# Kernel tuning notes

Measured on AMD Instinct MI355X. Metric: run time of the kernel, lower is better.

The kernel has to match this reference:

```python
import jax, jax.numpy as jnp
import numpy as np

N, D, E, TOP_K = 2048, 512, 16, 2
HID = 4 * D
EPS = 1e-10


def setup_inputs() -> dict:
    key = jax.random.key(0)
    ks = jax.random.split(key, 8)
    s = 0.02
    return {
        "x": jax.random.normal(ks[0], (N, D), dtype=jnp.float32),
        "w_norm": jnp.ones((D,), dtype=jnp.float32),
        "Wr": jax.random.normal(ks[1], (D, E), dtype=jnp.float32) * s,
        "br": jnp.zeros((E,), dtype=jnp.float32),
        "W1": jax.random.normal(ks[2], (E, D, HID), dtype=jnp.float32) * s,
        "b1": jnp.zeros((E, HID), dtype=jnp.float32),
        "W2": jax.random.normal(ks[3], (E, HID, D), dtype=jnp.float32) * s,
        "b2": jnp.zeros((E, D), dtype=jnp.float32),
    }


def reference(x, w_norm, Wr, br, W1, b1, W2, b2):
    res = x
    # RMSNorm over feature dim (dim=1 in the torch code for 2D input)
    rms = jnp.sqrt(jnp.mean(x * x, axis=1, keepdims=True) + EPS)
    xn = w_norm * (x / rms)
    # Router: top-k over expert logits, softmax over the k selected logits
    logits = xn @ Wr + br                      # [N, E]
    top_p, top_i = jax.lax.top_k(logits, TOP_K)  # [N, k]
    top_p = jax.nn.softmax(top_p, axis=-1)
    # Dense per-token expert weights [N, E] (top-k indices are distinct)
    weight = jnp.zeros((x.shape[0], E), dtype=x.dtype)
    weight = weight.at[jnp.arange(x.shape[0])[:, None], top_i].add(top_p)
    # All-expert FFN (dense reference for the routed dispatch)
    h = jnp.einsum("nd,edh->enh", xn, W1) + b1[:, None, :]   # [E, N, 4D]
    y = jnp.einsum("enh,ehd->end", jax.nn.silu(h), W2) + b2[:, None, :]  # [E, N, D]
    out = jnp.einsum("end,ne->nd", y, weight)
    return out + res
```

## Files before the change

kernel.cpp:

```cpp
#include <hip/hip_runtime.h>

#define N_TOK 2048
#define DIM   512
#define NEXP  16
#define HID   2048
#define NSLOT (N_TOK*2)

typedef __attribute__((ext_vector_type(8))) short short8;
typedef __attribute__((ext_vector_type(4))) float floatx4;

__device__ __forceinline__ ushort f2bf(float f) {
    union { float f; unsigned u; } c; c.f = f;
    unsigned u = c.u;
    unsigned r = (u + 0x7fffu + ((u >> 16) & 1u)) >> 16;
    return (ushort)r;
}

__device__ __forceinline__ void gl_lds16(const void* g, void* l) {
    __builtin_amdgcn_global_load_lds(
        (const __attribute__((address_space(1))) unsigned int*)g,
        (__attribute__((address_space(3))) unsigned int*)l, 16, 0, 0);
}

__global__ __launch_bounds__(256)
void transpose_convert(const float* __restrict__ src, ushort* __restrict__ dst,
                       int K, int Nn)
{
    const int NT = Nn >> 6, KT = K >> 6;
    int bx = blockIdx.x;
    const int nt = bx % NT; bx /= NT;
    const int kt = bx % KT; bx /= KT;
    const int e  = bx;

    __shared__ float Ls[64 * 65];
    const int t = threadIdx.x;

    const float* sp = src + ((size_t)e * K + kt * 64) * Nn + nt * 64;
#pragma unroll
    for (int i = 0; i < 4; i++) {
        const int k  = (t >> 4) + i * 16;
        const int c4 = (t & 15) * 4;
        const float4 v = *(const float4*)(sp + (size_t)k * Nn + c4);
        Ls[k * 65 + c4 + 0] = v.x;
        Ls[k * 65 + c4 + 1] = v.y;
        Ls[k * 65 + c4 + 2] = v.z;
        Ls[k * 65 + c4 + 3] = v.w;
    }
    __syncthreads();

    ushort* dp = dst + ((size_t)e * Nn + nt * 64) * K + kt * 64;
#pragma unroll
    for (int i = 0; i < 2; i++) {
        const int n = (t >> 3) + i * 32;
        const int c = t & 7;
        unsigned w[4];
#pragma unroll
        for (int q = 0; q < 4; q++) {
            const unsigned lo = f2bf(Ls[(c * 8 + q * 2 + 0) * 65 + n]);
            const unsigned hi = f2bf(Ls[(c * 8 + q * 2 + 1) * 65 + n]);
            w[q] = lo | (hi << 16);
        }
        uint4 o = make_uint4(w[0], w[1], w[2], w[3]);
        *(uint4*)(dp + (size_t)n * K + c * 8) = o;
    }
}

__global__ __launch_bounds__(256)
void router_fused(const float* __restrict__ x, const float* __restrict__ w_norm,
                  const float* __restrict__ Wr, const float* __restrict__ br,
                  ushort* __restrict__ xn, int2* __restrict__ rec_e,
                  float2* __restrict__ rec_w)
{
    __shared__ float xs[16][516];
    __shared__ float wrT[16][516];

    const int tid  = threadIdx.x;
    const int wave = tid >> 6, lane = tid & 63;
    const int tblk = blockIdx.x * 16;

#pragma unroll
    for (int k = 0; k < 32; k++) {
        const int idx = tid + k * 256;
        wrT[idx & 15][idx >> 4] = Wr[idx];
    }

    const float4* wnp = (const float4*)w_norm;
    const float4 wa = wnp[lane], wb = wnp[lane + 64];
#pragma unroll
    for (int i = 0; i < 4; i++) {
        const int tl = wave * 4 + i, t = tblk + tl;
        const float4* xp = (const float4*)(x + (size_t)t * DIM);
        const float4 a = xp[lane], b = xp[lane + 64];
        float ss = a.x*a.x + a.y*a.y + a.z*a.z + a.w*a.w
                 + b.x*b.x + b.y*b.y + b.z*b.z + b.w*b.w;
#pragma unroll
        for (int m = 32; m >= 1; m >>= 1) ss += __shfl_xor(ss, m, 64);
        const float rinv = 1.f / sqrtf(ss * (1.f / (float)DIM) + 1e-10f);
        float4 na, nb;
        na.x = a.x * wa.x * rinv; na.y = a.y * wa.y * rinv;
        na.z = a.z * wa.z * rinv; na.w = a.w * wa.w * rinv;
        nb.x = b.x * wb.x * rinv; nb.y = b.y * wb.y * rinv;
        nb.z = b.z * wb.z * rinv; nb.w = b.w * wb.w * rinv;
        *(float4*)&xs[tl][lane * 4]       = na;
        *(float4*)&xs[tl][256 + lane * 4] = nb;
        ushort4 ua, ub;
        ua.x = f2bf(na.x); ua.y = f2bf(na.y); ua.z = f2bf(na.z); ua.w = f2bf(na.w);
        ub.x = f2bf(nb.x); ub.y = f2bf(nb.y); ub.z = f2bf(nb.z); ub.w = f2bf(nb.w);
        ushort4* xo = (ushort4*)(xn + (size_t)t * DIM);
        xo[lane] = ua; xo[lane + 64] = ub;
    }
    __syncthreads();

    const int tl = tid >> 4, e = tid & 15;
    const int t = tblk + tl;
    float acc = 0.f;
#pragma unroll 4
    for (int d = 0; d < DIM; d += 4) {
        const float4 xv = *(const float4*)&xs[tl][d];
        const float4 wv = *(const float4*)&wrT[e][d];
        acc += xv.x * wv.x + xv.y * wv.y + xv.z * wv.z + xv.w * wv.w;
    }
    const float v = acc + br[e];

    float m0 = v; int i0 = e; float m1 = -1e30f; int i1 = 16;
#pragma unroll
    for (int msk = 1; msk < 16; msk <<= 1) {
        const float om0 = __shfl_xor(m0, msk, 64); const int oi0 = __shfl_xor(i0, msk, 64);
        const float om1 = __shfl_xor(m1, msk, 64); const int oi1 = __shfl_xor(i1, msk, 64);
        const bool bf_ = (om0 > m0) || (om0 == m0 && oi0 < i0);
        const float t0m = bf_ ? om0 : m0; const int t0i = bf_ ? oi0 : i0;
        const float l0m = bf_ ? m0 : om0; const int l0i = bf_ ? i0 : oi0;
        const bool b2_ = (om1 > m1) || (om1 == m1 && oi1 < i1);
        const float t2m = b2_ ? om1 : m1; const int t2i = b2_ ? oi1 : i1;
        const bool lw = (l0m > t2m) || (l0m == t2m && l0i < t2i);
        m0 = t0m; i0 = t0i;
        m1 = lw ? l0m : t2m; i1 = lw ? l0i : t2i;
    }
    if (e == 0) {
        const float ex = expf(m1 - m0);
        const float w0 = 1.f / (1.f + ex);
        rec_e[t] = make_int2(i0, i1);
        rec_w[t] = make_float2(w0, ex * w0);
    }
}

__global__ __launch_bounds__(1024)
void plan_kernel(const int2* __restrict__ rec_e, int* __restrict__ cnt,
                 int* __restrict__ off, int* __restrict__ tok_of_slot,
                 int* __restrict__ rec_slot)
{
    __shared__ int soff[17];
    const int e = threadIdx.x >> 6;
    const int lane = threadIdx.x & 63;

    int total = 0;
    for (int c = 0; c < N_TOK / 64; c++) {
        const int2 er = rec_e[c * 64 + lane];
        const bool hit = (er.x == e) || (er.y == e);
        total += __popcll(__ballot(hit));
    }
    if (lane == 0) soff[e + 1] = total;
    __syncthreads();
    if (threadIdx.x == 0) {
        soff[0] = 0;
        for (int q = 1; q <= 16; q++) soff[q] += soff[q - 1];
    }
    __syncthreads();
    int base = soff[e];
    if (lane == 0) { cnt[e] = soff[e + 1] - base; off[e] = base; }

    for (int c = 0; c < N_TOK / 64; c++) {
        const int t = c * 64 + lane;
        const int2 er = rec_e[t];
        const bool hit = (er.x == e) || (er.y == e);
        const unsigned long long b = __ballot(hit);
        if (hit) {
            const int slot = base + __popcll(b & ((1ull << lane) - 1ull));
            tok_of_slot[slot] = t;
            const int which = (er.y == e) ? 1 : 0;
            rec_slot[t * 2 + which] = slot;
        }
        base += __popcll(b);
    }
}

template<int MODE>
__global__ __launch_bounds__(512)
void gemm_expert(const ushort* __restrict__ A, int a_stride,
                 const ushort* __restrict__ WT, int wt_k,
                 const float* __restrict__ bias,
                 const int* __restrict__ cnt, const int* __restrict__ off,
                 const int* __restrict__ tok_of_slot,
                 ushort* __restrict__ hout, float* __restrict__ yout)
{
    const int flat = blockIdx.x + (blockIdx.y << 4);
    const int x = flat & 7;
    const int g = flat >> 3;
    int e, mt, nb, z;
    if (MODE == 0) {
        e  = x + ((g >> 6) << 3);
        const int r = g & 63;
        nb = r & 15; mt = r >> 4; z = 0;
    } else {
        const int G = ((g >> 4) << 3) + x;
        e = G >> 2; z = G & 3;
        const int idx = g & 15;
        mt = idx >> 2; nb = idx & 3;
    }

    const int count = cnt[e];
    if (mt * 128 >= count) return;
    const int base = off[e];
    const int rows = min(128, count - mt * 128);
    const int n0   = nb * 128;
    const int Nn   = (MODE == 0) ? HID : DIM;
    const int kbeg = (MODE == 0) ? 0 : (z * 512);
    float* yp = (MODE == 0) ? nullptr : (yout + (size_t)z * NSLOT * DIM);

    __shared__ __align__(16) ushort As[2][128 * 64];
    __shared__ __align__(16) ushort Bs[2][128 * 64];
    __shared__ int toks[128];

    const int tid = threadIdx.x;
    if (tid < 128) {
        const int r = tid < rows ? tid : rows - 1;
        const int slot = base + mt * 128 + r;
        toks[tid] = (MODE == 0) ? tok_of_slot[slot] : slot;
    }
    __syncthreads();

    const int lane = tid & 63;
    const int wid  = tid >> 6;
    const int wm = wid >> 2, wn = wid & 3;
    const int fr = lane & 15, fg = lane >> 4;

    const int lrow = lane >> 3;
    const int sch  = (lane & 7) ^ lrow;

    const ushort* aptr[2];
    const ushort* bptr[2];
    const ushort* wbase = WT + (size_t)e * Nn * wt_k + (size_t)n0 * wt_k;
#pragma unroll
    for (int j = 0; j < 2; j++) {
        const int s = wid * 2 + j;
        aptr[j] = A + (size_t)toks[s * 8 + lrow] * a_stride + sch * 8;
        bptr[j] = wbase + (size_t)(s * 8 + lrow) * wt_k + sch * 8;
    }

    floatx4 acc[4][2];
#pragma unroll
    for (int mi = 0; mi < 4; mi++)
#pragma unroll
        for (int ni = 0; ni < 2; ni++)
#pragma unroll
            for (int r = 0; r < 4; r++) acc[mi][ni][r] = 0.f;

#define STAGE(pb, k0)                                                        \
    do {                                                                     \
        _Pragma("unroll")                                                    \
        for (int j = 0; j < 2; j++)                                          \
            gl_lds16(aptr[j] + (k0), (void*)(&As[pb][(wid * 2 + j) * 512])); \
        _Pragma("unroll")                                                    \
        for (int j = 0; j < 2; j++)                                          \
            gl_lds16(bptr[j] + (k0), (void*)(&Bs[pb][(wid * 2 + j) * 512])); \
    } while (0)

    int cur = 0;
    STAGE(0, kbeg);

    for (int kt = 0; kt < 8; kt++) {
        if (kt < 7) {
            STAGE(cur ^ 1, kbeg + (kt + 1) * 64);
            asm volatile("s_waitcnt vmcnt(4)" ::: "memory");
        } else {
            asm volatile("s_waitcnt vmcnt(0)" ::: "memory");
        }
        __builtin_amdgcn_s_barrier();
        __builtin_amdgcn_sched_barrier(0);

        __builtin_amdgcn_s_setprio(1);
#pragma unroll
        for (int kh = 0; kh < 2; kh++) {
            const int co = ((kh * 4 + fg) ^ (fr & 7)) * 8;
            short8 af[4], bfr[2];
#pragma unroll
            for (int mi = 0; mi < 4; mi++)
                af[mi] = *(const short8*)&As[cur][(wm * 64 + mi * 16 + fr) * 64 + co];
#pragma unroll
            for (int ni = 0; ni < 2; ni++)
                bfr[ni] = *(const short8*)&Bs[cur][(wn * 32 + ni * 16 + fr) * 64 + co];
#pragma unroll
            for (int mi = 0; mi < 4; mi++)
#pragma unroll
                for (int ni = 0; ni < 2; ni++)
                    acc[mi][ni] = __builtin_amdgcn_mfma_f32_16x16x32_bf16(af[mi], bfr[ni], acc[mi][ni], 0, 0, 0);
        }
        __builtin_amdgcn_s_setprio(0);

        __builtin_amdgcn_sched_barrier(0);
        __builtin_amdgcn_s_barrier();
        cur ^= 1;
    }
#undef STAGE

#pragma unroll
    for (int ni = 0; ni < 2; ni++) {
        const int gn = n0 + wn * 32 + ni * 16 + fr;
        const float bv = (MODE == 0) ? bias[e * HID + gn] : 0.f;
#pragma unroll
        for (int mi = 0; mi < 4; mi++) {
#pragma unroll
            for (int r = 0; r < 4; r++) {
                const int lm = wm * 64 + mi * 16 + fg * 4 + r;
                if (lm < rows) {
                    const int slot = base + mt * 128 + lm;
                    float v = acc[mi][ni][r];
                    if (MODE == 0) {
                        v += bv;
                        v = v / (1.f + expf(-v));
                        hout[(size_t)slot * HID + gn] = f2bf(v);
                    } else {
                        yp[(size_t)slot * DIM + gn] = v;
                    }
                }
            }
        }
    }
}

__global__ __launch_bounds__(128)
void gather_kernel(const float* __restrict__ x, const float* __restrict__ ypart,
                   const float* __restrict__ b2,
                   const int2* __restrict__ rec_e, const float2* __restrict__ rec_w,
                   const int2* __restrict__ rec_slot, float* __restrict__ out)
{
    const int t = blockIdx.x;
    const int d4 = threadIdx.x * 4;
    const int2 ei = rec_e[t];
    const float2 w = rec_w[t];
    const int2 sl = rec_slot[t];
    const float4 xv  = *(const float4*)(x  + (size_t)t * DIM + d4);
    float4 s0 = make_float4(0.f, 0.f, 0.f, 0.f);
    float4 s1 = make_float4(0.f, 0.f, 0.f, 0.f);
#pragma unroll
    for (int kc = 0; kc < 4; kc++) {
        const float* yp = ypart + (size_t)kc * NSLOT * DIM;
        const float4 a = *(const float4*)(yp + (size_t)sl.x * DIM + d4);
        const float4 b = *(const float4*)(yp + (size_t)sl.y * DIM + d4);
        s0.x += a.x; s0.y += a.y; s0.z += a.z; s0.w += a.w;
        s1.x += b.x; s1.y += b.y; s1.z += b.z; s1.w += b.w;
    }
    const float4 b0  = *(const float4*)(b2 + (size_t)ei.x * DIM + d4);
    const float4 b1v = *(const float4*)(b2 + (size_t)ei.y * DIM + d4);
    float4 o;
    o.x = xv.x + w.x * (s0.x + b0.x) + w.y * (s1.x + b1v.x);
    o.y = xv.y + w.x * (s0.y + b0.y) + w.y * (s1.y + b1v.y);
    o.z = xv.z + w.x * (s0.z + b0.z) + w.y * (s1.z + b1v.z);
    o.w = xv.w + w.x * (s0.w + b0.w) + w.y * (s1.w + b1v.w);
    *(float4*)(out + (size_t)t * DIM + d4) = o;
}

extern "C" void kernel_launch(void* const* d_in, const int* in_sizes, int n_in,
                              void* d_out, int out_size, void* d_ws, size_t ws_size,
                              hipStream_t stream)
{
    const float* x  = (const float*)d_in[0];
    const float* wn = (const float*)d_in[1];
    const float* Wr = (const float*)d_in[2];
    const float* br = (const float*)d_in[3];
    const float* W1 = (const float*)d_in[4];
    const float* b1 = (const float*)d_in[5];
    const float* W2 = (const float*)d_in[6];
    const float* b2 = (const float*)d_in[7];
    float* out = (float*)d_out;

    char* ws = (char*)d_ws;
    ushort* W1T   = (ushort*)(ws);
    ushort* W2T   = (ushort*)(ws + (32u << 20));
    ushort* xn    = (ushort*)(ws + (64u << 20));
    ushort* h_buf = (ushort*)(ws + (66u << 20));
    float*  y_par = (float*) (ws + (82u << 20));
    char* p = ws + (114u << 20);
    int*    cnt         = (int*)p;    p += 256;
    int*    off         = (int*)p;    p += 256;
    int2*   rec_e       = (int2*)p;   p += N_TOK * 8;
    float2* rec_w       = (float2*)p; p += N_TOK * 8;
    int2*   rec_slot    = (int2*)p;   p += N_TOK * 8;
    int*    tok_of_slot = (int*)p;    p += NSLOT * 4;

    router_fused<<<N_TOK / 16, 256, 0, stream>>>(x, wn, Wr, br, xn, rec_e, rec_w);
    plan_kernel<<<1, 1024, 0, stream>>>(rec_e, cnt, off, tok_of_slot, (int*)rec_slot);

    transpose_convert<<<NEXP * 8 * 32, 256, 0, stream>>>(W1, W1T, DIM, HID);
    gemm_expert<0><<<dim3(16, 64), 512, 0, stream>>>(
        xn, DIM, W1T, DIM, b1, cnt, off, tok_of_slot, h_buf, nullptr);

    transpose_convert<<<NEXP * 32 * 8, 256, 0, stream>>>(W2, W2T, HID, DIM);
    gemm_expert<1><<<dim3(16, 64), 512, 0, stream>>>(
        h_buf, HID, W2T, HID, nullptr, cnt, off, nullptr, nullptr, y_par);

    gather_kernel<<<N_TOK, 128, 0, stream>>>(x, y_par, b2, rec_e, rec_w, rec_slot, out);
}
```

Before: 116.9 us.

## Double expert GEMM M-tile to 256 rows and store partial outputs in bf16

Expert GEMM blocks now cover 256 token rows instead of 128. Each wave computes a 64x64 sub-tile with a 4x4 MFMA accumulator array, and the grid is halved. The down-projection split-K partials are written as bf16 instead of fp32, and the gather kernel converts them back, which halves that intermediate traffic. SiLU switches to the fast __expf. The aim is better operand reuse and less memory traffic, at the cost of fewer active blocks, more LDS and registers per block, and slightly lower precision in the partial sums.

Result: slower. 126.8 us (+8.5%).

```diff
diff --git a/kernel.cpp b/kernel.cpp
--- a/kernel.cpp
+++ b/kernel.cpp
@@ -14,6 +14,10 @@
     unsigned u = c.u;
     unsigned r = (u + 0x7fffu + ((u >> 16) & 1u)) >> 16;
     return (ushort)r;
+}
+__device__ __forceinline__ float bf2f(ushort u) {
+    union { unsigned u; float f; } c; c.u = ((unsigned)u) << 16;
+    return c.f;
 }
 
 __device__ __forceinline__ void gl_lds16(const void* g, void* l) {
@@ -191,75 +195,79 @@
                  const float* __restrict__ bias,
                  const int* __restrict__ cnt, const int* __restrict__ off,
                  const int* __restrict__ tok_of_slot,
-                 ushort* __restrict__ hout, float* __restrict__ yout)
+                 ushort* __restrict__ hout, ushort* __restrict__ yout)
 {
     const int flat = blockIdx.x + (blockIdx.y << 4);
     const int x = flat & 7;
     const int g = flat >> 3;
     int e, mt, nb, z;
     if (MODE == 0) {
-        e  = x + ((g >> 6) << 3);
-        const int r = g & 63;
+        e  = x + ((g >> 5) << 3);
+        const int r = g & 31;
         nb = r & 15; mt = r >> 4; z = 0;
     } else {
-        const int G = ((g >> 4) << 3) + x;
+        const int G = ((g >> 3) << 3) + x;
         e = G >> 2; z = G & 3;
-        const int idx = g & 15;
+        const int idx = g & 7;
         mt = idx >> 2; nb = idx & 3;
     }
 
     const int count = cnt[e];
-    if (mt * 128 >= count) return;
+    if (mt * 256 >= count) return;
     const int base = off[e];
-    const int rows = min(128, count - mt * 128);
+    const int rows = min(256, count - mt * 256);
     const int n0   = nb * 128;
     const int Nn   = (MODE == 0) ? HID : DIM;
     const int kbeg = (MODE == 0) ? 0 : (z * 512);
-    float* yp = (MODE == 0) ? nullptr : (yout + (size_t)z * NSLOT * DIM);
-
-    __shared__ __align__(16) ushort As[2][128 * 64];
+    ushort* yp = (MODE == 0) ? nullptr : (yout + (size_t)z * NSLOT * DIM);
+
+    __shared__ __align__(16) ushort As[2][256 * 64];
     __shared__ __align__(16) ushort Bs[2][128 * 64];
-    __shared__ int toks[128];
+    __shared__ int toks[256];
 
     const int tid = threadIdx.x;
-    if (tid < 128) {
+    if (tid < 256) {
         const int r = tid < rows ? tid : rows - 1;
-        const int slot = base + mt * 128 + r;
+        const int slot = base + mt * 256 + r;
         toks[tid] = (MODE == 0) ? tok_of_slot[slot] : slot;
     }
     __syncthreads();
 
     const int lane = tid & 63;
     const int wid  = tid >> 6;
-    const int wm = wid >> 2, wn = wid & 3;
+    const int wm = wid >> 1, wn = wid & 1;
     const int fr = lane & 15, fg = lane >> 4;
 
     const int lrow = lane >> 3;
     const int sch  = (lane & 7) ^ lrow;
 
-    const ushort* aptr[2];
+    const ushort* aptr[4];
     const ushort* bptr[2];
     const ushort* wbase = WT + (size_t)e * Nn * wt_k + (size_t)n0 * wt_k;
 #pragma unroll
+    for (int j = 0; j < 4; j++) {
+        const int s = wid * 4 + j;
+        aptr[j] = A + (size_t)toks[s * 8 + lrow] * a_stride + sch * 8;
+    }
+#pragma unroll
     for (int j = 0; j < 2; j++) {
         const int s = wid * 2 + j;
-        aptr[j] = A + (size_t)toks[s * 8 + lrow] * a_stride + sch * 8;
         bptr[j] = wbase + (size_t)(s * 8 + lrow) * wt_k + sch * 8;
     }
 
-    floatx4 acc[4][2];
+    floatx4 acc[4][4];
 #pragma unroll
     for (int mi = 0; mi < 4; mi++)
 #pragma unroll
-        for (int ni = 0; ni < 2; ni++)
+        for (int ni = 0; ni < 4; ni++)
 #pragma unroll
             for (int r = 0; r < 4; r++) acc[mi][ni][r] = 0.f;
 
 #define STAGE(pb, k0)                                                        \
     do {                                                                     \
         _Pragma("unroll")                                                    \
-        for (int j = 0; j < 2; j++)                                          \
-            gl_lds16(aptr[j] + (k0), (void*)(&As[pb][(wid * 2 + j) * 512])); \
+        for (int j = 0; j < 4; j++)                                          \
+            gl_lds16(aptr[j] + (k0), (void*)(&As[pb][(wid * 4 + j) * 512])); \
         _Pragma("unroll")                                                    \
         for (int j = 0; j < 2; j++)                                          \
             gl_lds16(bptr[j] + (k0), (void*)(&Bs[pb][(wid * 2 + j) * 512])); \
@@ -271,7 +279,7 @@
     for (int kt = 0; kt < 8; kt++) {
         if (kt < 7) {
             STAGE(cur ^ 1, kbeg + (kt + 1) * 64);
-            asm volatile("s_waitcnt vmcnt(4)" ::: "memory");
+            asm volatile("s_waitcnt vmcnt(6)" ::: "memory");
         } else {
             asm volatile("s_waitcnt vmcnt(0)" ::: "memory");
         }
@@ -282,17 +290,17 @@
 #pragma unroll
         for (int kh = 0; kh < 2; kh++) {
             const int co = ((kh * 4 + fg) ^ (fr & 7)) * 8;
-            short8 af[4], bfr[2];
+            short8 af[4], bfr[4];
 #pragma unroll
             for (int mi = 0; mi < 4; mi++)
                 af[mi] = *(const short8*)&As[cur][(wm * 64 + mi * 16 + fr) * 64 + co];
 #pragma unroll
-            for (int ni = 0; ni < 2; ni++)
-                bfr[ni] = *(const short8*)&Bs[cur][(wn * 32 + ni * 16 + fr) * 64 + co];
+            for (int ni = 0; ni < 4; ni++)
+                bfr[ni] = *(const short8*)&Bs[cur][(wn * 64 + ni * 16 + fr) * 64 + co];
 #pragma unroll
             for (int mi = 0; mi < 4; mi++)
 #pragma unroll
-                for (int ni = 0; ni < 2; ni++)
+                for (int ni = 0; ni < 4; ni++)
                     acc[mi][ni] = __builtin_amdgcn_mfma_f32_16x16x32_bf16(af[mi], bfr[ni], acc[mi][ni], 0, 0, 0);
         }
         __builtin_amdgcn_s_setprio(0);
@@ -304,8 +312,8 @@
 #undef STAGE
 
 #pragma unroll
-    for (int ni = 0; ni < 2; ni++) {
-        const int gn = n0 + wn * 32 + ni * 16 + fr;
+    for (int ni = 0; ni < 4; ni++) {
+        const int gn = n0 + wn * 64 + ni * 16 + fr;
         const float bv = (MODE == 0) ? bias[e * HID + gn] : 0.f;
 #pragma unroll
         for (int mi = 0; mi < 4; mi++) {
@@ -313,14 +321,14 @@
             for (int r = 0; r < 4; r++) {
                 const int lm = wm * 64 + mi * 16 + fg * 4 + r;
                 if (lm < rows) {
-                    const int slot = base + mt * 128 + lm;
+                    const int slot = base + mt * 256 + lm;
                     float v = acc[mi][ni][r];
                     if (MODE == 0) {
                         v += bv;
-                        v = v / (1.f + expf(-v));
+                        v = v / (1.f + __expf(-v));
                         hout[(size_t)slot * HID + gn] = f2bf(v);
                     } else {
-                        yp[(size_t)slot * DIM + gn] = v;
+                        yp[(size_t)slot * DIM + gn] = f2bf(v);
                     }
                 }
             }
@@ -329,7 +337,7 @@
 }
 
 __global__ __launch_bounds__(128)
-void gather_kernel(const float* __restrict__ x, const float* __restrict__ ypart,
+void gather_kernel(const float* __restrict__ x, const ushort* __restrict__ ypart,
                    const float* __restrict__ b2,
                    const int2* __restrict__ rec_e, const float2* __restrict__ rec_w,
                    const int2* __restrict__ rec_slot, float* __restrict__ out)
@@ -344,11 +352,11 @@
     float4 s1 = make_float4(0.f, 0.f, 0.f, 0.f);
 #pragma unroll
     for (int kc = 0; kc < 4; kc++) {
-        const float* yp = ypart + (size_t)kc * NSLOT * DIM;
-        const float4 a = *(const float4*)(yp + (size_t)sl.x * DIM + d4);
-        const float4 b = *(const float4*)(yp + (size_t)sl.y * DIM + d4);
-        s0.x += a.x; s0.y += a.y; s0.z += a.z; s0.w += a.w;
-        s1.x += b.x; s1.y += b.y; s1.z += b.z; s1.w += b.w;
+        const ushort* yp = ypart + (size_t)kc * NSLOT * DIM;
+        const ushort4 a = *(const ushort4*)(yp + (size_t)sl.x * DIM + d4);
+        const ushort4 b = *(const ushort4*)(yp + (size_t)sl.y * DIM + d4);
+        s0.x += bf2f(a.x); s0.y += bf2f(a.y); s0.z += bf2f(a.z); s0.w += bf2f(a.w);
+        s1.x += bf2f(b.x); s1.y += bf2f(b.y); s1.z += bf2f(b.z); s1.w += bf2f(b.w);
     }
     const float4 b0  = *(const float4*)(b2 + (size_t)ei.x * DIM + d4);
     const float4 b1v = *(const float4*)(b2 + (size_t)ei.y * DIM + d4);
@@ -379,7 +387,7 @@
     ushort* W2T   = (ushort*)(ws + (32u << 20));
     ushort* xn    = (ushort*)(ws + (64u << 20));
     ushort* h_buf = (ushort*)(ws + (66u << 20));
-    float*  y_par = (float*) (ws + (82u << 20));
+    ushort* y_par = (ushort*)(ws + (82u << 20));
     char* p = ws + (114u << 20);
     int*    cnt         = (int*)p;    p += 256;
     int*    off         = (int*)p;    p += 256;
@@ -392,11 +400,11 @@
     plan_kernel<<<1, 1024, 0, stream>>>(rec_e, cnt, off, tok_of_slot, (int*)rec_slot);
 
     transpose_convert<<<NEXP * 8 * 32, 256, 0, stream>>>(W1, W1T, DIM, HID);
-    gemm_expert<0><<<dim3(16, 64), 512, 0, stream>>>(
+    gemm_expert<0><<<dim3(16, 32), 512, 0, stream>>>(
         xn, DIM, W1T, DIM, b1, cnt, off, tok_of_slot, h_buf, nullptr);
 
     transpose_convert<<<NEXP * 32 * 8, 256, 0, stream>>>(W2, W2T, HID, DIM);
-    gemm_expert<1><<<dim3(16, 64), 512, 0, stream>>>(
+    gemm_expert<1><<<dim3(16, 32), 512, 0, stream>>>(
         h_buf, HID, W2T, HID, nullptr, cnt, off, nullptr, nullptr, y_par);
 
     gather_kernel<<<N_TOK, 128, 0, stream>>>(x, y_par, b2, rec_e, rec_w, rec_slot, out);
```
